# Kernel optimization log

Hardware: AMD Instinct MI355X
Metric: run time of the kernel (lower is better)

Reference implementation:

```python
import jax, jax.numpy as jnp
import numpy as np

N = 100000
E = 500000
IN, HID, OUT = 128, 256, 128


def _graph_conv(x, src, dst, W, b, n):
    # dgl GraphConv with norm='both': D_dst^-1/2 * A * D_src^-1/2 * x @ W + b
    ones = jnp.ones(src.shape[0], dtype=x.dtype)
    deg_out = jnp.clip(jax.ops.segment_sum(ones, src, num_segments=n), 1.0)
    deg_in = jnp.clip(jax.ops.segment_sum(ones, dst, num_segments=n), 1.0)
    c_src = deg_out ** -0.5
    c_dst = deg_in ** -0.5
    msg = x[src] * c_src[src][:, None]            # [E, F] gather + scale
    agg = jax.ops.segment_sum(msg, dst, num_segments=n) * c_dst[:, None]
    return agg @ W + b


def setup_inputs() -> dict:
    key = jax.random.key(0)
    ks = jax.random.split(key, 20)
    d = {
        'x': jax.random.normal(ks[0], (N, IN), dtype=jnp.float32),
        'src_b': jax.random.randint(ks[1], (E,), 0, N),
        'dst_b': jax.random.randint(ks[2], (E,), 0, N),
        'src_r': jax.random.randint(ks[3], (E,), 0, N),
        'dst_r': jax.random.randint(ks[4], (E,), 0, N),
        'src_j': jax.random.randint(ks[5], (E,), 0, N),
        'dst_j': jax.random.randint(ks[6], (E,), 0, N),
    }
    s1 = 1.0 / np.sqrt(IN)
    s2 = 1.0 / np.sqrt(HID)
    for i, r in enumerate(['b', 'r', 'j']):
        d[f'W1_{r}'] = jax.random.normal(ks[7 + i], (IN, HID), dtype=jnp.float32) * s1
        d[f'b1_{r}'] = jnp.zeros((HID,), dtype=jnp.float32)
        d[f'W2_{r}'] = jax.random.normal(ks[10 + i], (HID, OUT), dtype=jnp.float32) * s2
        d[f'b2_{r}'] = jnp.zeros((OUT,), dtype=jnp.float32)
    return d


def reference(x, src_b, dst_b, src_r, dst_r, src_j, dst_j,
              W1_b, b1_b, W1_r, b1_r, W1_j, b1_j,
              W2_b, b2_b, W2_r, b2_r, W2_j, b2_j):
    n = x.shape[0]
    edges = {'b': (src_b, dst_b), 'r': (src_r, dst_r), 'j': (src_j, dst_j)}
    W1 = {'b': (W1_b, b1_b), 'r': (W1_r, b1_r), 'j': (W1_j, b1_j)}
    W2 = {'b': (W2_b, b2_b), 'r': (W2_r, b2_r), 'j': (W2_j, b2_j)}
    # layer 1: sum over relations (HeteroGraphConv default aggregate='sum')
    h = sum(_graph_conv(x, edges[r][0], edges[r][1], W1[r][0], W1[r][1], n)
            for r in ('b', 'r', 'j'))
    h = jax.nn.relu(h)
    out = sum(_graph_conv(h, edges[r][0], edges[r][1], W2[r][0], W2[r][1], n)
              for r in ('b', 'r', 'j'))
    return out
```

## Files before the change

kernel.cpp:

```cpp
#include <hip/hip_runtime.h>
#include <hip/hip_bf16.h>
#include <cstdint>

#define NNODE 100000
#define NEDGE 500000
#define FIN   128
#define FHID  256
#define FOUT  128

#define NBUCK  1563
#define CHUNK  2048
#define NCHUNK 245

typedef __attribute__((ext_vector_type(8))) short bf16x8;
typedef __attribute__((ext_vector_type(4))) float f32x4;


__device__ inline unsigned short f2bf(float f) {
    unsigned int u = __float_as_uint(f);
    unsigned int r = (u + 0x7FFF + ((u >> 16) & 1)) >> 16;
    return (unsigned short)r;
}
__device__ inline float bf2f(unsigned short s) {
    return __uint_as_float(((unsigned int)s) << 16);
}
__device__ inline void split2(float f, unsigned short& hi, unsigned short& lo) {
    hi = f2bf(f);
    lo = f2bf(f - bf2f(hi));
}


__global__ __launch_bounds__(256)
void csr_count(const int* __restrict__ sb, const int* __restrict__ db,
               const int* __restrict__ sr, const int* __restrict__ dr,
               const int* __restrict__ sj, const int* __restrict__ dj,
               int* __restrict__ bh_dst, int* __restrict__ bh_src) {
    __shared__ int h1[NBUCK], h2[NBUCK];
    const int r = blockIdx.y, c = blockIdx.x, tid = threadIdx.x;
    const int* s = (r == 0) ? sb : (r == 1) ? sr : sj;
    const int* d = (r == 0) ? db : (r == 1) ? dr : dj;
    for (int i = tid; i < NBUCK; i += 256) { h1[i] = 0; h2[i] = 0; }
    __syncthreads();
    const int e0 = c * CHUNK;
#pragma unroll
    for (int i = 0; i < CHUNK / 256; ++i) {
        int e = e0 + i * 256 + tid;
        if (e < NEDGE) {
            atomicAdd(&h1[d[e] >> 6], 1);
            atomicAdd(&h2[s[e] >> 6], 1);
        }
    }
    __syncthreads();
    int* o1 = bh_dst + ((size_t)r * NCHUNK + c) * NBUCK;
    int* o2 = bh_src + ((size_t)r * NCHUNK + c) * NBUCK;
    for (int i = tid; i < NBUCK; i += 256) { o1[i] = h1[i]; o2[i] = h2[i]; }
}

__global__ void csr_scan_chunks(int* __restrict__ bh_dst, int* __restrict__ bh_src,
                                int* __restrict__ tot) {
    int idx = blockIdx.x * blockDim.x + threadIdx.x;
    if (idx >= 2 * 3 * NBUCK) return;
    int k = idx / (3 * NBUCK);
    int rem = idx - k * 3 * NBUCK;
    int r = rem / NBUCK;
    int b = rem - r * NBUCK;
    int* p = ((k == 0) ? bh_dst : bh_src) + (size_t)r * NCHUNK * NBUCK + b;
    int t = 0;
    int c = 0;
    for (; c + 4 <= NCHUNK; c += 4) {
        int v0 = p[0], v1 = p[NBUCK], v2 = p[2 * NBUCK], v3 = p[3 * NBUCK];
        p[0] = t; t += v0;
        p[NBUCK] = t; t += v1;
        p[2 * NBUCK] = t; t += v2;
        p[3 * NBUCK] = t; t += v3;
        p += 4 * NBUCK;
    }
    for (; c < NCHUNK; ++c) { int v = *p; *p = t; t += v; p += NBUCK; }
    tot[(k * 3 + r) * NBUCK + b] = t;
}

__global__ void csr_scan_buckets(const int* __restrict__ tot, int* __restrict__ bb) {
    const int k = blockIdx.x, r = blockIdx.y, tid = threadIdx.x;
    const int base_in = (k * 3 + r) * NBUCK;
    const int base_out = (k * 3 + r) * (NBUCK + 1);
    int v[8];
    const int idx0 = tid * 8;
    int tsum = 0;
#pragma unroll
    for (int i = 0; i < 8; ++i) {
        int ii = idx0 + i;
        v[i] = (ii < NBUCK) ? tot[base_in + ii] : 0;
        tsum += v[i];
    }
    __shared__ int sm[256];
    sm[tid] = tsum;
    __syncthreads();
    for (int off = 1; off < 256; off <<= 1) {
        int t = 0;
        if (tid >= off) t = sm[tid - off];
        __syncthreads();
        sm[tid] += t;
        __syncthreads();
    }
    int run = sm[tid] - tsum;
#pragma unroll
    for (int i = 0; i < 8; ++i) {
        int ii = idx0 + i;
        if (ii <= NBUCK) bb[base_out + ii] = run;
        run += v[i];
    }
}

__global__ __launch_bounds__(256)
void csr_scatter(const int* __restrict__ sb, const int* __restrict__ db,
                 const int* __restrict__ sr, const int* __restrict__ dr,
                 const int* __restrict__ sj, const int* __restrict__ dj,
                 const int* __restrict__ bh_dst, const int* __restrict__ bh_src,
                 const int* __restrict__ bb, unsigned int* __restrict__ ebd,
                 unsigned char* __restrict__ ebs) {
    __shared__ int cur1[NBUCK], cur2[NBUCK];
    const int r = blockIdx.y, c = blockIdx.x, tid = threadIdx.x;
    const int* s = (r == 0) ? sb : (r == 1) ? sr : sj;
    const int* d = (r == 0) ? db : (r == 1) ? dr : dj;
    const int* p1 = bh_dst + ((size_t)r * NCHUNK + c) * NBUCK;
    const int* p2 = bh_src + ((size_t)r * NCHUNK + c) * NBUCK;
    const int* bb1 = bb + r * (NBUCK + 1);
    const int* bb2 = bb + (3 + r) * (NBUCK + 1);
    for (int i = tid; i < NBUCK; i += 256) {
        cur1[i] = bb1[i] + p1[i];
        cur2[i] = bb2[i] + p2[i];
    }
    __syncthreads();
    const int e0 = c * CHUNK;
#pragma unroll
    for (int i = 0; i < CHUNK / 256; ++i) {
        int e = e0 + i * 256 + tid;
        if (e < NEDGE) {
            int dv = d[e], sv = s[e];
            int q1 = atomicAdd(&cur1[dv >> 6], 1);
            ebd[(size_t)r * NEDGE + q1] = ((unsigned)(dv & 63) << 17) | (unsigned)sv;
            int q2 = atomicAdd(&cur2[sv >> 6], 1);
            ebs[(size_t)r * NEDGE + q2] = (unsigned char)(sv & 63);
        }
    }
}

__global__ __launch_bounds__(256)
void csr_finalize_dst(const unsigned int* __restrict__ ebd, const int* __restrict__ bb,
                      int* __restrict__ cnt_dst, int* __restrict__ rp,
                      int* __restrict__ col) {
    __shared__ int hist[64], pref[64], cur[64];
    const int b = blockIdx.x, r = blockIdx.y, tid = threadIdx.x;
    const int* bb1 = bb + r * (NBUCK + 1);
    const int seg0 = bb1[b], seg1 = bb1[b + 1];
    if (tid < 64) hist[tid] = 0;
    __syncthreads();
    const unsigned int* eb = ebd + (size_t)r * NEDGE;
    for (int e = seg0 + tid; e < seg1; e += 256)
        atomicAdd(&hist[eb[e] >> 17], 1);
    __syncthreads();
    if (tid == 0) {
        int run = 0;
        for (int i = 0; i < 64; ++i) { pref[i] = run; run += hist[i]; }
    }
    __syncthreads();
    if (tid < 64) {
        int node = b * 64 + tid;
        if (node < NNODE) {
            cnt_dst[r * NNODE + node] = hist[tid];
            rp[r * (NNODE + 1) + node] = seg0 + pref[tid];
        }
        cur[tid] = seg0 + pref[tid];
    }
    if (b == 0 && tid == 0) rp[r * (NNODE + 1) + NNODE] = NEDGE;
    __syncthreads();
    for (int e = seg0 + tid; e < seg1; e += 256) {
        unsigned int key = eb[e];
        int pos = atomicAdd(&cur[key >> 17], 1);
        col[(size_t)r * NEDGE + pos] = (int)(key & 0x1FFFF);
    }
}

__global__ __launch_bounds__(256)
void csr_count_src(const unsigned char* __restrict__ ebs, const int* __restrict__ bbs,
                   int* __restrict__ cnt_src) {
    __shared__ int hist[64];
    const int b = blockIdx.x, r = blockIdx.y, tid = threadIdx.x;
    const int* bb2 = bbs + r * (NBUCK + 1);
    const int seg0 = bb2[b], seg1 = bb2[b + 1];
    if (tid < 64) hist[tid] = 0;
    __syncthreads();
    const unsigned char* eb = ebs + (size_t)r * NEDGE;
    for (int e = seg0 + tid; e < seg1; e += 256)
        atomicAdd(&hist[eb[e]], 1);
    __syncthreads();
    if (tid < 64) {
        int node = b * 64 + tid;
        if (node < NNODE) cnt_src[r * NNODE + node] = hist[tid];
    }
}


__global__ void norms_kernel(const int* __restrict__ cnt_src, const int* __restrict__ cnt_dst,
                             float* __restrict__ c_src, float* __restrict__ c_dst) {
    int i = blockIdx.x * blockDim.x + threadIdx.x;
    if (i >= 3 * NNODE) return;
    c_src[i] = rsqrtf((float)max(cnt_src[i], 1));
    c_dst[i] = rsqrtf((float)max(cnt_dst[i], 1));
}

__global__ void bias_sums(const float* __restrict__ b1b, const float* __restrict__ b1r,
                          const float* __restrict__ b1j, const float* __restrict__ b2b,
                          const float* __restrict__ b2r, const float* __restrict__ b2j,
                          float* __restrict__ b1s, float* __restrict__ b2s) {
    int i = threadIdx.x;
    if (i < FHID) b1s[i] = b1b[i] + b1r[i] + b1j[i];
    if (i < FOUT) b2s[i] = b2b[i] + b2r[i] + b2j[i];
}

__global__ void x2bf_kernel(const float4* __restrict__ x4, ushort4* __restrict__ xb4, int n4) {
    int i = blockIdx.x * blockDim.x + threadIdx.x;
    if (i >= n4) return;
    float4 v = x4[i];
    ushort4 o;
    o.x = f2bf(v.x);
    o.y = f2bf(v.y);
    o.z = f2bf(v.z);
    o.w = f2bf(v.w);
    xb4[i] = o;
}

__global__ void wsplit_t(const float* __restrict__ W, unsigned short* __restrict__ th,
                         unsigned short* __restrict__ tl, int K, int N, int ldt,
                         int nbase, int kbase) {
    int i = blockIdx.x * blockDim.x + threadIdx.x;
    if (i >= K * N) return;
    int k = i / N;
    int n = i - k * N;
    unsigned short hi, lo;
    split2(W[i], hi, lo);
    size_t o = (size_t)(nbase + n) * ldt + kbase + k;
    th[o] = hi;
    tl[o] = lo;
}


__device__ inline void gather_chunk(const ushort2* __restrict__ rows, int ldrow,
                                    const int* __restrict__ colp,
                                    const float* __restrict__ csrc, int e0, int e1,
                                    int lane, float& ax, float& ay) {
    for (int base = e0; base < e1; base += 64) {
        int cnt = min(64, e1 - base);
        int sl = (lane < cnt) ? colp[base + lane] : 0;
        float wl = (lane < cnt) ? csrc[sl] : 0.f;
        int j = 0;
        for (; j + 4 <= cnt; j += 4) {
            int s0 = __shfl(sl, j), s1 = __shfl(sl, j + 1);
            int s2 = __shfl(sl, j + 2), s3 = __shfl(sl, j + 3);
            float w0 = __shfl(wl, j), w1 = __shfl(wl, j + 1);
            float w2 = __shfl(wl, j + 2), w3 = __shfl(wl, j + 3);
            ushort2 v0 = rows[(size_t)s0 * ldrow + lane];
            ushort2 v1 = rows[(size_t)s1 * ldrow + lane];
            ushort2 v2 = rows[(size_t)s2 * ldrow + lane];
            ushort2 v3 = rows[(size_t)s3 * ldrow + lane];
            ax += w0 * bf2f(v0.x); ay += w0 * bf2f(v0.y);
            ax += w1 * bf2f(v1.x); ay += w1 * bf2f(v1.y);
            ax += w2 * bf2f(v2.x); ay += w2 * bf2f(v2.y);
            ax += w3 * bf2f(v3.x); ay += w3 * bf2f(v3.y);
        }
        for (; j < cnt; ++j) {
            int s = __shfl(sl, j);
            float w = __shfl(wl, j);
            ushort2 v = rows[(size_t)s * ldrow + lane];
            ax += w * bf2f(v.x); ay += w * bf2f(v.y);
        }
    }
}

__global__ __launch_bounds__(256)
void spmm1_all(const ushort2* __restrict__ xb, const int* __restrict__ rp,
               const int* __restrict__ col, const float* __restrict__ c_src,
               const float* __restrict__ c_dst, ushort2* __restrict__ agg) {
    int wid = (blockIdx.x * blockDim.x + threadIdx.x) >> 6;
    int lane = threadIdx.x & 63;
    if (wid >= NNODE) return;
    int e0[3], e1[3], sl[3];
    float wl[3];
#pragma unroll
    for (int r = 0; r < 3; ++r) {
        e0[r] = rp[r * (NNODE + 1) + wid];
        e1[r] = rp[r * (NNODE + 1) + wid + 1];
    }
#pragma unroll
    for (int r = 0; r < 3; ++r) {
        int cnt = min(e1[r] - e0[r], 64);
        sl[r] = (lane < cnt) ? col[r * NEDGE + e0[r] + lane] : 0;
    }
#pragma unroll
    for (int r = 0; r < 3; ++r) {
        int cnt = min(e1[r] - e0[r], 64);
        wl[r] = (lane < cnt) ? c_src[r * NNODE + sl[r]] : 0.f;
    }
#pragma unroll
    for (int r = 0; r < 3; ++r) {
        float ax = 0.f, ay = 0.f;
        int cnt = min(e1[r] - e0[r], 64);
        int j = 0;
        for (; j + 4 <= cnt; j += 4) {
            int s0 = __shfl(sl[r], j), s1 = __shfl(sl[r], j + 1);
            int s2 = __shfl(sl[r], j + 2), s3 = __shfl(sl[r], j + 3);
            float w0 = __shfl(wl[r], j), w1 = __shfl(wl[r], j + 1);
            float w2 = __shfl(wl[r], j + 2), w3 = __shfl(wl[r], j + 3);
            ushort2 v0 = xb[(size_t)s0 * (FIN / 2) + lane];
            ushort2 v1 = xb[(size_t)s1 * (FIN / 2) + lane];
            ushort2 v2 = xb[(size_t)s2 * (FIN / 2) + lane];
            ushort2 v3 = xb[(size_t)s3 * (FIN / 2) + lane];
            ax += w0 * bf2f(v0.x); ay += w0 * bf2f(v0.y);
            ax += w1 * bf2f(v1.x); ay += w1 * bf2f(v1.y);
            ax += w2 * bf2f(v2.x); ay += w2 * bf2f(v2.y);
            ax += w3 * bf2f(v3.x); ay += w3 * bf2f(v3.y);
        }
        for (; j < cnt; ++j) {
            int s = __shfl(sl[r], j);
            float w = __shfl(wl[r], j);
            ushort2 v = xb[(size_t)s * (FIN / 2) + lane];
            ax += w * bf2f(v.x); ay += w * bf2f(v.y);
        }
        if (e0[r] + 64 < e1[r])
            gather_chunk(xb, FIN / 2, col + (size_t)r * NEDGE, c_src + r * NNODE,
                         e0[r] + 64, e1[r], lane, ax, ay);
        float cd = c_dst[r * NNODE + wid];
        ushort2 o;
        o.x = f2bf(ax * cd);
        o.y = f2bf(ay * cd);
        agg[(size_t)wid * (3 * FIN / 2) + r * (FIN / 2) + lane] = o;
    }
}

__global__ __launch_bounds__(256)
void spmm2_all(const ushort2* __restrict__ yb, const int* __restrict__ rp,
               const int* __restrict__ col, const float* __restrict__ c_src,
               const float* __restrict__ c_dst, const float2* __restrict__ b2s2,
               float2* __restrict__ out2) {
    int wid = (blockIdx.x * blockDim.x + threadIdx.x) >> 6;
    int lane = threadIdx.x & 63;
    if (wid >= NNODE) return;
    int e0[3], e1[3], sl[3];
    float wl[3];
#pragma unroll
    for (int r = 0; r < 3; ++r) {
        e0[r] = rp[r * (NNODE + 1) + wid];
        e1[r] = rp[r * (NNODE + 1) + wid + 1];
    }
#pragma unroll
    for (int r = 0; r < 3; ++r) {
        int cnt = min(e1[r] - e0[r], 64);
        sl[r] = (lane < cnt) ? col[r * NEDGE + e0[r] + lane] : 0;
    }
#pragma unroll
    for (int r = 0; r < 3; ++r) {
        int cnt = min(e1[r] - e0[r], 64);
        wl[r] = (lane < cnt) ? c_src[r * NNODE + sl[r]] : 0.f;
    }
    float2 acc = b2s2[lane];
#pragma unroll
    for (int r = 0; r < 3; ++r) {
        const ushort2* rows = yb + r * (FOUT / 2);
        float ax = 0.f, ay = 0.f;
        int cnt = min(e1[r] - e0[r], 64);
        int j = 0;
        for (; j + 4 <= cnt; j += 4) {
            int s0 = __shfl(sl[r], j), s1 = __shfl(sl[r], j + 1);
            int s2 = __shfl(sl[r], j + 2), s3 = __shfl(sl[r], j + 3);
            float w0 = __shfl(wl[r], j), w1 = __shfl(wl[r], j + 1);
            float w2 = __shfl(wl[r], j + 2), w3 = __shfl(wl[r], j + 3);
            ushort2 v0 = rows[(size_t)s0 * (3 * FOUT / 2) + lane];
            ushort2 v1 = rows[(size_t)s1 * (3 * FOUT / 2) + lane];
            ushort2 v2 = rows[(size_t)s2 * (3 * FOUT / 2) + lane];
            ushort2 v3 = rows[(size_t)s3 * (3 * FOUT / 2) + lane];
            ax += w0 * bf2f(v0.x); ay += w0 * bf2f(v0.y);
            ax += w1 * bf2f(v1.x); ay += w1 * bf2f(v1.y);
            ax += w2 * bf2f(v2.x); ay += w2 * bf2f(v2.y);
            ax += w3 * bf2f(v3.x); ay += w3 * bf2f(v3.y);
        }
        for (; j < cnt; ++j) {
            int s = __shfl(sl[r], j);
            float w = __shfl(wl[r], j);
            ushort2 v = rows[(size_t)s * (3 * FOUT / 2) + lane];
            ax += w * bf2f(v.x); ay += w * bf2f(v.y);
        }
        if (e0[r] + 64 < e1[r])
            gather_chunk(rows, 3 * FOUT / 2, col + (size_t)r * NEDGE, c_src + r * NNODE,
                         e0[r] + 64, e1[r], lane, ax, ay);
        float cd = c_dst[r * NNODE + wid];
        acc.x += cd * ax;
        acc.y += cd * ay;
    }
    out2[(size_t)wid * (FOUT / 2) + lane] = acc;
}


template <int K, int EPI>
__global__ __launch_bounds__(256)
void gemm_bf16(const unsigned short* __restrict__ A, const unsigned short* __restrict__ Bh,
               const unsigned short* __restrict__ Bl, const float* __restrict__ bias,
               unsigned short* __restrict__ C, int M, int N) {
    __shared__ unsigned short As[128][40];
    __shared__ unsigned short Bsh[128][40];
    __shared__ unsigned short Bsl[128][40];
    const int bm = blockIdx.x * 128;
    const int bn = blockIdx.y * 128;
    const int tid = threadIdx.x;
    const int lane = tid & 63;
    const int wv = tid >> 6;
    const int wm = (wv >> 1) * 64;
    const int wn = (wv & 1) * 64;

    const int srow = tid >> 1;
    const int scol = (tid & 1) * 16;
    const size_t abase = (size_t)(bm + srow) * K + scol;
    const size_t bbase = (size_t)(bn + srow) * K + scol;
    const bool avalid = (bm + srow) < M;

    f32x4 acc[4][4] = {};

    for (int k0 = 0; k0 < K; k0 += 32) {
        uint4 z = make_uint4(0, 0, 0, 0);
        uint4 a0 = z, a1 = z;
        if (avalid) {
            a0 = *(const uint4*)&A[abase + k0];
            a1 = *(const uint4*)&A[abase + k0 + 8];
        }
        uint4 b0 = *(const uint4*)&Bh[bbase + k0];
        uint4 b1 = *(const uint4*)&Bh[bbase + k0 + 8];
        uint4 m0 = *(const uint4*)&Bl[bbase + k0];
        uint4 m1 = *(const uint4*)&Bl[bbase + k0 + 8];
        *(uint4*)&As[srow][scol] = a0;
        *(uint4*)&As[srow][scol + 8] = a1;
        *(uint4*)&Bsh[srow][scol] = b0;
        *(uint4*)&Bsh[srow][scol + 8] = b1;
        *(uint4*)&Bsl[srow][scol] = m0;
        *(uint4*)&Bsl[srow][scol + 8] = m1;
        __syncthreads();

        const int kb = (lane >> 4) * 8;
        const int fr = lane & 15;
        bf16x8 a[4], bh[4], bl[4];
#pragma unroll
        for (int i = 0; i < 4; ++i) {
            a[i] = *(const bf16x8*)&As[wm + i * 16 + fr][kb];
            bh[i] = *(const bf16x8*)&Bsh[wn + i * 16 + fr][kb];
            bl[i] = *(const bf16x8*)&Bsl[wn + i * 16 + fr][kb];
        }
#pragma unroll
        for (int mi = 0; mi < 4; ++mi)
#pragma unroll
            for (int ni = 0; ni < 4; ++ni) {
                acc[mi][ni] = __builtin_amdgcn_mfma_f32_16x16x32_bf16(a[mi], bh[ni], acc[mi][ni], 0, 0, 0);
                acc[mi][ni] = __builtin_amdgcn_mfma_f32_16x16x32_bf16(a[mi], bl[ni], acc[mi][ni], 0, 0, 0);
            }
        __syncthreads();
    }

    const int cl = lane & 15;
    const int rl = (lane >> 4) * 4;
#pragma unroll
    for (int mi = 0; mi < 4; ++mi) {
#pragma unroll
        for (int ni = 0; ni < 4; ++ni) {
            const int gcol = bn + wn + ni * 16 + cl;
            float bv = (EPI == 0) ? bias[gcol] : 0.f;
#pragma unroll
            for (int rg = 0; rg < 4; ++rg) {
                const int grow = bm + wm + mi * 16 + rl + rg;
                if (grow < M) {
                    float v = acc[mi][ni][rg];
                    if (EPI == 0) v = fmaxf(v + bv, 0.f);
                    C[(size_t)grow * N + gcol] = f2bf(v);
                }
            }
        }
    }
}


extern "C" void kernel_launch(void* const* d_in, const int* in_sizes, int n_in,
                              void* d_out, int out_size, void* d_ws, size_t ws_size,
                              hipStream_t stream) {
    const float* x = (const float*)d_in[0];
    const int* src_b = (const int*)d_in[1];
    const int* dst_b = (const int*)d_in[2];
    const int* src_r = (const int*)d_in[3];
    const int* dst_r = (const int*)d_in[4];
    const int* src_j = (const int*)d_in[5];
    const int* dst_j = (const int*)d_in[6];
    const float* W1[3] = {(const float*)d_in[7], (const float*)d_in[11], (const float*)d_in[15]};
    const float* b1[3] = {(const float*)d_in[8], (const float*)d_in[12], (const float*)d_in[16]};
    const float* W2[3] = {(const float*)d_in[9], (const float*)d_in[13], (const float*)d_in[17]};
    const float* b2[3] = {(const float*)d_in[10], (const float*)d_in[14], (const float*)d_in[18]};
    float* out = (float*)d_out;

    char* w = (char*)d_ws;
    auto alloc = [&](size_t bytes) -> char* {
        char* p = w;
        w += (bytes + 255) & ~(size_t)255;
        return p;
    };
    int* cnt = (int*)alloc((size_t)6 * NNODE * 4);
    int* cnt_src = cnt;
    int* cnt_dst = cnt + 3 * NNODE;
    float* c_src = (float*)alloc((size_t)3 * NNODE * 4);
    float* c_dst = (float*)alloc((size_t)3 * NNODE * 4);
    int* rp = (int*)alloc((size_t)3 * (NNODE + 1) * 4);
    int* tot = (int*)alloc((size_t)2 * 3 * NBUCK * 4);
    int* bb = (int*)alloc((size_t)2 * 3 * (NBUCK + 1) * 4);
    int* col = (int*)alloc((size_t)3 * NEDGE * 4);
    float* b1s = (float*)alloc(FHID * 4);
    float* b2s = (float*)alloc(FOUT * 4);
    unsigned short* xbf = (unsigned short*)alloc((size_t)NNODE * FIN * 2);
    unsigned short* aggcat = (unsigned short*)alloc((size_t)NNODE * 3 * FIN * 2);
    unsigned short* ycat = aggcat;
    unsigned short* hb = (unsigned short*)alloc((size_t)NNODE * FHID * 2);

    char* sc = (char*)aggcat;
    int* bh_dst = (int*)sc;                          sc += (size_t)3 * NCHUNK * NBUCK * 4;
    int* bh_src = (int*)sc;                          sc += (size_t)3 * NCHUNK * NBUCK * 4;
    unsigned int* ebd = (unsigned int*)sc;           sc += (size_t)3 * NEDGE * 4;
    unsigned char* ebs = (unsigned char*)sc;         sc += (size_t)3 * NEDGE;

    unsigned short* w1h = (unsigned short*)cnt;
    unsigned short* w1l = w1h + FHID * 3 * FIN;
    unsigned short* w2h = w1l + FHID * 3 * FIN;
    unsigned short* w2l = w2h + 3 * FOUT * FHID;

    const int T = 256;

    csr_count<<<dim3(NCHUNK, 3), T, 0, stream>>>(
        src_b, dst_b, src_r, dst_r, src_j, dst_j, bh_dst, bh_src);
    csr_scan_chunks<<<dim3((2 * 3 * NBUCK + T - 1) / T), T, 0, stream>>>(bh_dst, bh_src, tot);
    csr_scan_buckets<<<dim3(2, 3), T, 0, stream>>>(tot, bb);
    csr_scatter<<<dim3(NCHUNK, 3), T, 0, stream>>>(
        src_b, dst_b, src_r, dst_r, src_j, dst_j, bh_dst, bh_src, bb, ebd, ebs);
    csr_finalize_dst<<<dim3(NBUCK, 3), T, 0, stream>>>(ebd, bb, cnt_dst, rp, col);
    csr_count_src<<<dim3(NBUCK, 3), T, 0, stream>>>(ebs, bb + 3 * (NBUCK + 1), cnt_src);
    norms_kernel<<<dim3((3 * NNODE + T - 1) / T), T, 0, stream>>>(cnt_src, cnt_dst, c_src, c_dst);

    x2bf_kernel<<<dim3((NNODE * FIN / 4 + T - 1) / T), T, 0, stream>>>(
        (const float4*)x, (ushort4*)xbf, NNODE * FIN / 4);
    for (int r = 0; r < 3; ++r) {
        wsplit_t<<<dim3((FIN * FHID + T - 1) / T), T, 0, stream>>>(
            W1[r], w1h, w1l, FIN, FHID, 3 * FIN, 0, r * FIN);
        wsplit_t<<<dim3((FHID * FOUT + T - 1) / T), T, 0, stream>>>(
            W2[r], w2h, w2l, FHID, FOUT, FHID, r * FOUT, 0);
    }
    bias_sums<<<1, 256, 0, stream>>>(b1[0], b1[1], b1[2], b2[0], b2[1], b2[2], b1s, b2s);

    const dim3 spmm_grid((NNODE * 64 + T - 1) / T);

    spmm1_all<<<spmm_grid, T, 0, stream>>>(
        (const ushort2*)xbf, rp, col, c_src, c_dst, (ushort2*)aggcat);
    gemm_bf16<3 * FIN, 0><<<dim3((NNODE + 127) / 128, FHID / 128), 256, 0, stream>>>(
        aggcat, w1h, w1l, b1s, hb, NNODE, FHID);

    gemm_bf16<FHID, 1><<<dim3((NNODE + 127) / 128, (3 * FOUT) / 128), 256, 0, stream>>>(
        hb, w2h, w2l, nullptr, ycat, NNODE, 3 * FOUT);
    spmm2_all<<<spmm_grid, T, 0, stream>>>(
        (const ushort2*)ycat, rp, col, c_src, c_dst, (const float2*)b2s, (float2*)out);
}
```

Measured before the change: 534.0 us.

## Fuse CSR finalize with src counting and norms, merge prep kernels, 8-wide gather

Merges the dst finalize, src degree counting and norm computation into one kernel that writes c_src/c_dst directly. It also folds the x-to-bf16 conversion, the six weight split/transpose launches and the bias sums into one prep kernel. The gather loop is unrolled eight-wide, with masked weights replacing the scalar tail. This cuts kernel launches and the intermediate count buffers, at the cost of extra masked loads on short rows.

```diff
diff --git a/kernel.cpp b/kernel.cpp
--- a/kernel.cpp
+++ b/kernel.cpp
@@ -146,12 +146,13 @@
 }
 
 __global__ __launch_bounds__(256)
-void csr_finalize_dst(const unsigned int* __restrict__ ebd, const int* __restrict__ bb,
-                      int* __restrict__ cnt_dst, int* __restrict__ rp,
-                      int* __restrict__ col) {
+void csr_finalize(const unsigned int* __restrict__ ebd, const unsigned char* __restrict__ ebs,
+                  const int* __restrict__ bb, int* __restrict__ rp, int* __restrict__ col,
+                  float* __restrict__ c_src, float* __restrict__ c_dst) {
     __shared__ int hist[64], pref[64], cur[64];
     const int b = blockIdx.x, r = blockIdx.y, tid = threadIdx.x;
     const int* bb1 = bb + r * (NBUCK + 1);
+    const int* bb2 = bb + (3 + r) * (NBUCK + 1);
     const int seg0 = bb1[b], seg1 = bb1[b + 1];
     if (tid < 64) hist[tid] = 0;
     __syncthreads();
@@ -167,8 +168,8 @@
     if (tid < 64) {
         int node = b * 64 + tid;
         if (node < NNODE) {
-            cnt_dst[r * NNODE + node] = hist[tid];
             rp[r * (NNODE + 1) + node] = seg0 + pref[tid];
+            c_dst[r * NNODE + node] = rsqrtf((float)max(hist[tid], 1));
         }
         cur[tid] = seg0 + pref[tid];
     }
@@ -179,71 +180,93 @@
         int pos = atomicAdd(&cur[key >> 17], 1);
         col[(size_t)r * NEDGE + pos] = (int)(key & 0x1FFFF);
     }
-}
-
-__global__ __launch_bounds__(256)
-void csr_count_src(const unsigned char* __restrict__ ebs, const int* __restrict__ bbs,
-                   int* __restrict__ cnt_src) {
-    __shared__ int hist[64];
-    const int b = blockIdx.x, r = blockIdx.y, tid = threadIdx.x;
-    const int* bb2 = bbs + r * (NBUCK + 1);
-    const int seg0 = bb2[b], seg1 = bb2[b + 1];
+    __syncthreads();
     if (tid < 64) hist[tid] = 0;
     __syncthreads();
-    const unsigned char* eb = ebs + (size_t)r * NEDGE;
-    for (int e = seg0 + tid; e < seg1; e += 256)
-        atomicAdd(&hist[eb[e]], 1);
+    const int t0 = bb2[b], t1 = bb2[b + 1];
+    const unsigned char* es = ebs + (size_t)r * NEDGE;
+    for (int e = t0 + tid; e < t1; e += 256)
+        atomicAdd(&hist[es[e]], 1);
     __syncthreads();
     if (tid < 64) {
         int node = b * 64 + tid;
-        if (node < NNODE) cnt_src[r * NNODE + node] = hist[tid];
-    }
-}
-
-
-__global__ void norms_kernel(const int* __restrict__ cnt_src, const int* __restrict__ cnt_dst,
-                             float* __restrict__ c_src, float* __restrict__ c_dst) {
-    int i = blockIdx.x * blockDim.x + threadIdx.x;
-    if (i >= 3 * NNODE) return;
-    c_src[i] = rsqrtf((float)max(cnt_src[i], 1));
-    c_dst[i] = rsqrtf((float)max(cnt_dst[i], 1));
-}
-
-__global__ void bias_sums(const float* __restrict__ b1b, const float* __restrict__ b1r,
-                          const float* __restrict__ b1j, const float* __restrict__ b2b,
-                          const float* __restrict__ b2r, const float* __restrict__ b2j,
-                          float* __restrict__ b1s, float* __restrict__ b2s) {
-    int i = threadIdx.x;
-    if (i < FHID) b1s[i] = b1b[i] + b1r[i] + b1j[i];
-    if (i < FOUT) b2s[i] = b2b[i] + b2r[i] + b2j[i];
-}
-
-__global__ void x2bf_kernel(const float4* __restrict__ x4, ushort4* __restrict__ xb4, int n4) {
-    int i = blockIdx.x * blockDim.x + threadIdx.x;
-    if (i >= n4) return;
-    float4 v = x4[i];
-    ushort4 o;
-    o.x = f2bf(v.x);
-    o.y = f2bf(v.y);
-    o.z = f2bf(v.z);
-    o.w = f2bf(v.w);
-    xb4[i] = o;
-}
-
-__global__ void wsplit_t(const float* __restrict__ W, unsigned short* __restrict__ th,
-                         unsigned short* __restrict__ tl, int K, int N, int ldt,
-                         int nbase, int kbase) {
-    int i = blockIdx.x * blockDim.x + threadIdx.x;
-    if (i >= K * N) return;
-    int k = i / N;
-    int n = i - k * N;
-    unsigned short hi, lo;
-    split2(W[i], hi, lo);
-    size_t o = (size_t)(nbase + n) * ldt + kbase + k;
-    th[o] = hi;
-    tl[o] = lo;
-}
-
+        if (node < NNODE) c_src[r * NNODE + node] = rsqrtf((float)max(hist[tid], 1));
+    }
+}
+
+#define XB_BLOCKS 12500
+
+__global__ __launch_bounds__(256)
+void prep_all(const float4* __restrict__ x4, ushort4* __restrict__ xb4,
+              const float* __restrict__ W10, const float* __restrict__ W11,
+              const float* __restrict__ W12, const float* __restrict__ W20,
+              const float* __restrict__ W21, const float* __restrict__ W22,
+              const float* __restrict__ b10, const float* __restrict__ b11,
+              const float* __restrict__ b12, const float* __restrict__ b20,
+              const float* __restrict__ b21, const float* __restrict__ b22,
+              unsigned short* __restrict__ w1h, unsigned short* __restrict__ w1l,
+              unsigned short* __restrict__ w2h, unsigned short* __restrict__ w2l,
+              float* __restrict__ b1s, float* __restrict__ b2s) {
+    int b = blockIdx.x;
+    const int tid = threadIdx.x;
+    if (b < XB_BLOCKS) {
+        int i = b * 256 + tid;
+        float4 v = x4[i];
+        ushort4 o;
+        o.x = f2bf(v.x); o.y = f2bf(v.y); o.z = f2bf(v.z); o.w = f2bf(v.w);
+        xb4[i] = o;
+        return;
+    }
+    b -= XB_BLOCKS;
+    if (b < 768) {
+        int task = b >> 7;
+        int i = ((b & 127) << 8) | tid;
+        const float* W;
+        unsigned short *th, *tl;
+        int N, ldt, nbase, kbase;
+        if (task < 3) {
+            W = (task == 0) ? W10 : (task == 1) ? W11 : W12;
+            th = w1h; tl = w1l; N = FHID; ldt = 3 * FIN; nbase = 0; kbase = task * FIN;
+        } else {
+            int r = task - 3;
+            W = (r == 0) ? W20 : (r == 1) ? W21 : W22;
+            th = w2h; tl = w2l; N = FOUT; ldt = FHID; nbase = r * FOUT; kbase = 0;
+        }
+        int k = i / N;
+        int n = i - k * N;
+        unsigned short hi, lo;
+        split2(W[i], hi, lo);
+        size_t o = (size_t)(nbase + n) * ldt + kbase + k;
+        th[o] = hi;
+        tl[o] = lo;
+        return;
+    }
+    if (tid < FHID) b1s[tid] = b10[tid] + b11[tid] + b12[tid];
+    if (tid < FOUT) b2s[tid] = b20[tid] + b21[tid] + b22[tid];
+}
+
+
+__device__ inline void gather8(const ushort2* __restrict__ rows, int ldrow,
+                               int sl, float wl, int cnt, int lane,
+                               float& ax, float& ay) {
+    for (int j = 0; j < cnt; j += 8) {
+        float w[8];
+        ushort2 v[8];
+#pragma unroll
+        for (int u = 0; u < 8; ++u) {
+            int jj = (j + u) & 63;
+            int s = __shfl(sl, jj);
+            float ww = __shfl(wl, jj);
+            w[u] = (j + u < cnt) ? ww : 0.f;
+            v[u] = rows[(size_t)s * ldrow + lane];
+        }
+#pragma unroll
+        for (int u = 0; u < 8; ++u) {
+            ax += w[u] * bf2f(v[u].x);
+            ay += w[u] * bf2f(v[u].y);
+        }
+    }
+}
 
 __device__ inline void gather_chunk(const ushort2* __restrict__ rows, int ldrow,
                                     const int* __restrict__ colp,
@@ -253,27 +276,7 @@
         int cnt = min(64, e1 - base);
         int sl = (lane < cnt) ? colp[base + lane] : 0;
         float wl = (lane < cnt) ? csrc[sl] : 0.f;
-        int j = 0;
-        for (; j + 4 <= cnt; j += 4) {
-            int s0 = __shfl(sl, j), s1 = __shfl(sl, j + 1);
-            int s2 = __shfl(sl, j + 2), s3 = __shfl(sl, j + 3);
-            float w0 = __shfl(wl, j), w1 = __shfl(wl, j + 1);
-            float w2 = __shfl(wl, j + 2), w3 = __shfl(wl, j + 3);
-            ushort2 v0 = rows[(size_t)s0 * ldrow + lane];
-            ushort2 v1 = rows[(size_t)s1 * ldrow + lane];
-            ushort2 v2 = rows[(size_t)s2 * ldrow + lane];
-            ushort2 v3 = rows[(size_t)s3 * ldrow + lane];
-            ax += w0 * bf2f(v0.x); ay += w0 * bf2f(v0.y);
-            ax += w1 * bf2f(v1.x); ay += w1 * bf2f(v1.y);
-            ax += w2 * bf2f(v2.x); ay += w2 * bf2f(v2.y);
-            ax += w3 * bf2f(v3.x); ay += w3 * bf2f(v3.y);
-        }
-        for (; j < cnt; ++j) {
-            int s = __shfl(sl, j);
-            float w = __shfl(wl, j);
-            ushort2 v = rows[(size_t)s * ldrow + lane];
-            ax += w * bf2f(v.x); ay += w * bf2f(v.y);
-        }
+        gather8(rows, ldrow, sl, wl, cnt, lane, ax, ay);
     }
 }
 
@@ -305,27 +308,7 @@
     for (int r = 0; r < 3; ++r) {
         float ax = 0.f, ay = 0.f;
         int cnt = min(e1[r] - e0[r], 64);
-        int j = 0;
-        for (; j + 4 <= cnt; j += 4) {
-            int s0 = __shfl(sl[r], j), s1 = __shfl(sl[r], j + 1);
-            int s2 = __shfl(sl[r], j + 2), s3 = __shfl(sl[r], j + 3);
-            float w0 = __shfl(wl[r], j), w1 = __shfl(wl[r], j + 1);
-            float w2 = __shfl(wl[r], j + 2), w3 = __shfl(wl[r], j + 3);
-            ushort2 v0 = xb[(size_t)s0 * (FIN / 2) + lane];
-            ushort2 v1 = xb[(size_t)s1 * (FIN / 2) + lane];
-            ushort2 v2 = xb[(size_t)s2 * (FIN / 2) + lane];
-            ushort2 v3 = xb[(size_t)s3 * (FIN / 2) + lane];
-            ax += w0 * bf2f(v0.x); ay += w0 * bf2f(v0.y);
-            ax += w1 * bf2f(v1.x); ay += w1 * bf2f(v1.y);
-            ax += w2 * bf2f(v2.x); ay += w2 * bf2f(v2.y);
-            ax += w3 * bf2f(v3.x); ay += w3 * bf2f(v3.y);
-        }
-        for (; j < cnt; ++j) {
-            int s = __shfl(sl[r], j);
-            float w = __shfl(wl[r], j);
-            ushort2 v = xb[(size_t)s * (FIN / 2) + lane];
-            ax += w * bf2f(v.x); ay += w * bf2f(v.y);
-        }
+        gather8(xb, FIN / 2, sl[r], wl[r], cnt, lane, ax, ay);
         if (e0[r] + 64 < e1[r])
             gather_chunk(xb, FIN / 2, col + (size_t)r * NEDGE, c_src + r * NNODE,
                          e0[r] + 64, e1[r], lane, ax, ay);
@@ -368,27 +351,7 @@
         const ushort2* rows = yb + r * (FOUT / 2);
         float ax = 0.f, ay = 0.f;
         int cnt = min(e1[r] - e0[r], 64);
-        int j = 0;
-        for (; j + 4 <= cnt; j += 4) {
-            int s0 = __shfl(sl[r], j), s1 = __shfl(sl[r], j + 1);
-            int s2 = __shfl(sl[r], j + 2), s3 = __shfl(sl[r], j + 3);
-            float w0 = __shfl(wl[r], j), w1 = __shfl(wl[r], j + 1);
-            float w2 = __shfl(wl[r], j + 2), w3 = __shfl(wl[r], j + 3);
-            ushort2 v0 = rows[(size_t)s0 * (3 * FOUT / 2) + lane];
-            ushort2 v1 = rows[(size_t)s1 * (3 * FOUT / 2) + lane];
-            ushort2 v2 = rows[(size_t)s2 * (3 * FOUT / 2) + lane];
-            ushort2 v3 = rows[(size_t)s3 * (3 * FOUT / 2) + lane];
-            ax += w0 * bf2f(v0.x); ay += w0 * bf2f(v0.y);
-            ax += w1 * bf2f(v1.x); ay += w1 * bf2f(v1.y);
-            ax += w2 * bf2f(v2.x); ay += w2 * bf2f(v2.y);
-            ax += w3 * bf2f(v3.x); ay += w3 * bf2f(v3.y);
-        }
-        for (; j < cnt; ++j) {
-            int s = __shfl(sl[r], j);
-            float w = __shfl(wl[r], j);
-            ushort2 v = rows[(size_t)s * (3 * FOUT / 2) + lane];
-            ax += w * bf2f(v.x); ay += w * bf2f(v.y);
-        }
+        gather8(rows, 3 * FOUT / 2, sl[r], wl[r], cnt, lane, ax, ay);
         if (e0[r] + 64 < e1[r])
             gather_chunk(rows, 3 * FOUT / 2, col + (size_t)r * NEDGE, c_src + r * NNODE,
                          e0[r] + 64, e1[r], lane, ax, ay);
@@ -506,9 +469,6 @@
         w += (bytes + 255) & ~(size_t)255;
         return p;
     };
-    int* cnt = (int*)alloc((size_t)6 * NNODE * 4);
-    int* cnt_src = cnt;
-    int* cnt_dst = cnt + 3 * NNODE;
     float* c_src = (float*)alloc((size_t)3 * NNODE * 4);
     float* c_dst = (float*)alloc((size_t)3 * NNODE * 4);
     int* rp = (int*)alloc((size_t)3 * (NNODE + 1) * 4);
@@ -517,21 +477,21 @@
     int* col = (int*)alloc((size_t)3 * NEDGE * 4);
     float* b1s = (float*)alloc(FHID * 4);
     float* b2s = (float*)alloc(FOUT * 4);
+    unsigned short* wpl = (unsigned short*)alloc((size_t)4 * 98304 * 2);
+    unsigned short* w1h = wpl;
+    unsigned short* w1l = w1h + FHID * 3 * FIN;
+    unsigned short* w2h = w1l + FHID * 3 * FIN;
+    unsigned short* w2l = w2h + 3 * FOUT * FHID;
     unsigned short* xbf = (unsigned short*)alloc((size_t)NNODE * FIN * 2);
     unsigned short* aggcat = (unsigned short*)alloc((size_t)NNODE * 3 * FIN * 2);
     unsigned short* ycat = aggcat;
     unsigned short* hb = (unsigned short*)alloc((size_t)NNODE * FHID * 2);
 
     char* sc = (char*)aggcat;
-    int* bh_dst = (int*)sc;                          sc += (size_t)3 * NCHUNK * NBUCK * 4;
-    int* bh_src = (int*)sc;                          sc += (size_t)3 * NCHUNK * NBUCK * 4;
-    unsigned int* ebd = (unsigned int*)sc;           sc += (size_t)3 * NEDGE * 4;
-    unsigned char* ebs = (unsigned char*)sc;         sc += (size_t)3 * NEDGE;
-
-    unsigned short* w1h = (unsigned short*)cnt;
-    unsigned short* w1l = w1h + FHID * 3 * FIN;
-    unsigned short* w2h = w1l + FHID * 3 * FIN;
-    unsigned short* w2l = w2h + 3 * FOUT * FHID;
+    int* bh_dst = (int*)sc;                  sc += (size_t)3 * NCHUNK * NBUCK * 4;
+    int* bh_src = (int*)sc;                  sc += (size_t)3 * NCHUNK * NBUCK * 4;
+    unsigned int* ebd = (unsigned int*)sc;   sc += (size_t)3 * NEDGE * 4;
+    unsigned char* ebs = (unsigned char*)sc; sc += (size_t)3 * NEDGE;
 
     const int T = 256;
 
@@ -541,19 +501,13 @@
     csr_scan_buckets<<<dim3(2, 3), T, 0, stream>>>(tot, bb);
     csr_scatter<<<dim3(NCHUNK, 3), T, 0, stream>>>(
         src_b, dst_b, src_r, dst_r, src_j, dst_j, bh_dst, bh_src, bb, ebd, ebs);
-    csr_finalize_dst<<<dim3(NBUCK, 3), T, 0, stream>>>(ebd, bb, cnt_dst, rp, col);
-    csr_count_src<<<dim3(NBUCK, 3), T, 0, stream>>>(ebs, bb + 3 * (NBUCK + 1), cnt_src);
-    norms_kernel<<<dim3((3 * NNODE + T - 1) / T), T, 0, stream>>>(cnt_src, cnt_dst, c_src, c_dst);
-
-    x2bf_kernel<<<dim3((NNODE * FIN / 4 + T - 1) / T), T, 0, stream>>>(
-        (const float4*)x, (ushort4*)xbf, NNODE * FIN / 4);
-    for (int r = 0; r < 3; ++r) {
-        wsplit_t<<<dim3((FIN * FHID + T - 1) / T), T, 0, stream>>>(
-            W1[r], w1h, w1l, FIN, FHID, 3 * FIN, 0, r * FIN);
-        wsplit_t<<<dim3((FHID * FOUT + T - 1) / T), T, 0, stream>>>(
-            W2[r], w2h, w2l, FHID, FOUT, FHID, r * FOUT, 0);
-    }
-    bias_sums<<<1, 256, 0, stream>>>(b1[0], b1[1], b1[2], b2[0], b2[1], b2[2], b1s, b2s);
+    csr_finalize<<<dim3(NBUCK, 3), T, 0, stream>>>(ebd, ebs, bb, rp, col, c_src, c_dst);
+
+    prep_all<<<dim3(XB_BLOCKS + 768 + 1), T, 0, stream>>>(
+        (const float4*)x, (ushort4*)xbf,
+        W1[0], W1[1], W1[2], W2[0], W2[1], W2[2],
+        b1[0], b1[1], b1[2], b2[0], b2[1], b2[2],
+        w1h, w1l, w2h, w2l, b1s, b2s);
 
     const dim3 spmm_grid((NNODE * 64 + T - 1) / T);
 
```

After: 487.5 us. 1.1x faster.
